# Performance work log

Hardware: AMD Instinct MI355X
Metric: run time of the kernel (lower is better)

Reference implementation:

```python
import jax, jax.numpy as jnp
import numpy as np

NUM_HEADS = 12
HEAD_SIZE = 64  # hidden_size // num_heads


def setup_inputs() -> dict:
    key = jax.random.key(0)
    ks = jax.random.split(key, 4)
    B, S, H = 2, 2048, 768
    return {
        "hidden_states": jax.random.normal(ks[0], (B, S, H), dtype=jnp.float32),
        "attention_mask": jnp.ones((B, S), dtype=jnp.int32),
        "Wq": jax.random.normal(ks[1], (H, H), dtype=jnp.float32) * 0.02,
        "bq": jnp.zeros((H,), dtype=jnp.float32),
        "Wk": jax.random.normal(ks[2], (H, H), dtype=jnp.float32) * 0.02,
        "bk": jnp.zeros((H,), dtype=jnp.float32),
        "Wv": jax.random.normal(ks[3], (H, H), dtype=jnp.float32) * 0.02,
        "bv": jnp.zeros((H,), dtype=jnp.float32),
    }


def reference(hidden_states, attention_mask, Wq, bq, Wk, bk, Wv, bv):
    B, S, H = hidden_states.shape
    nh, hs = NUM_HEADS, HEAD_SIZE

    def to_heads(x):  # [B,S,H] -> [nh,B,S,hs] (matches to_multi_head)
        return x.reshape(B, S, nh, hs).transpose(2, 0, 1, 3)

    # torch Linear: y = x @ W.T + b
    q = to_heads(hidden_states @ Wq.T + bq)
    k = to_heads(hidden_states @ Wk.T + bk)
    v = to_heads(hidden_states @ Wv.T + bv)

    scores = jnp.einsum("hbqd,hbkd->hbqk", q, k) / jnp.float32(hs) ** 0.5
    # mask: 1 -> attend, 0 -> -inf; broadcast over query dim
    m = 1.0 - attention_mask.astype(scores.dtype)
    add = jnp.where(m != 0.0, -jnp.inf, 0.0)[None, :, None, :]  # [1,B,1,S]
    probs = jax.nn.softmax(scores + add, axis=-1)
    # dropout is identity in eval mode
    out = jnp.einsum("hbqk,hbkd->hbqd", probs, v)
    # from_multi_head: [nh,B,S,hs] -> [B,S,H]
    return out.transpose(1, 2, 0, 3).reshape(B, S, H)
```

## Files before the change

### kernel.cpp

```cpp
#include <hip/hip_runtime.h>
#include <hip/hip_bf16.h>

#define BATCH 2
#define SEQ   2048
#define HID   768
#define NH    12
#define HS    64
#define MROWS (BATCH*SEQ)
#define N3    (3*HID)
#define HB    (NH*BATCH)

typedef __attribute__((ext_vector_type(8))) short short8;
typedef __attribute__((ext_vector_type(4))) float floatx4;

#define QSCALE 0.1803368801111204f

__device__ __forceinline__ unsigned short f2bf(float x){
  __hip_bfloat16 h = __float2bfloat16(x);
  return __builtin_bit_cast(unsigned short, h);
}
__device__ __forceinline__ unsigned int f2bf2(float lo, float hi){
  return (unsigned int)f2bf(lo) | ((unsigned int)f2bf(hi) << 16);
}
__device__ __forceinline__ void glds16(const unsigned short* g, unsigned short* l){
  __builtin_amdgcn_global_load_lds(
    (const __attribute__((address_space(1))) unsigned int*)g,
    (__attribute__((address_space(3))) unsigned int*)l, 16, 0, 0);
}
#define WAITCNT_VM_LGKM0() __builtin_amdgcn_s_waitcnt(0x0070)

__global__ void f2bf_all_kernel(const float* __restrict__ X,
                                const float* __restrict__ Wq,
                                const float* __restrict__ Wk,
                                const float* __restrict__ Wv,
                                const int* __restrict__ mask,
                                unsigned short* __restrict__ Xb,
                                unsigned short* __restrict__ Wb,
                                float* __restrict__ maskaddG,
                                unsigned int* __restrict__ flagsG){
  const int XQ = MROWS*HID/4;
  const int WQ = HID*HID/4;
  const int NB = (XQ + 3*WQ)/256;
  const int tid = threadIdx.x;
  if(blockIdx.x == NB){
    for(int i=tid;i<BATCH*SEQ;i+=256) maskaddG[i] = mask[i] ? 0.f : -1e30f;
    if(tid < 2) flagsG[tid] = 0u;
    __syncthreads();
    if(tid < BATCH*32){
      int b = tid >> 5, t = tid & 31;
      const int* mrow = mask + b*SEQ + t*64;
      int any = 0;
      for(int i=0;i<64;i++) any |= (mrow[i]==0);
      if(any) atomicOr(&flagsG[b], 1u << t);
    }
    return;
  }
  int i = blockIdx.x * 256 + tid;
  const float* src; unsigned short* dst; int off;
  if(i < XQ){ src = X; dst = Xb; off = i; }
  else {
    int j = i - XQ;
    int w = j / WQ; off = j - w*WQ;
    src = (w==0) ? Wq : (w==1) ? Wk : Wv;
    dst = Wb + (size_t)w*HID*HID;
  }
  float4 v = reinterpret_cast<const float4*>(src)[off];
  ushort4 o;
  o.x = f2bf(v.x); o.y = f2bf(v.y); o.z = f2bf(v.z); o.w = f2bf(v.w);
  reinterpret_cast<ushort4*>(dst)[off] = o;
}

__global__ __launch_bounds__(256) void qkv_gemm_kernel(
    const unsigned short* __restrict__ Xb,
    const unsigned short* __restrict__ Wb,
    const float* __restrict__ bq, const float* __restrict__ bk, const float* __restrict__ bv,
    unsigned short* __restrict__ Qb, unsigned short* __restrict__ Kb,
    unsigned short* __restrict__ Vtb)
{
  __shared__ __align__(16) union {
    struct { unsigned short A[2][128][32]; unsigned short B[2][128][32]; } s;
    unsigned short T[4][64][72];
  } u;
  const int m0 = blockIdx.y << 7;
  const int n0 = blockIdx.x << 7;
  const int tid  = threadIdx.x;
  const int wave = tid >> 6, lane = tid & 63;
  const int wr = wave >> 1, wc = wave & 1;
  const int quad = lane >> 4, l15 = lane & 15;

  const unsigned short* gsrc[4];
  unsigned short* ldst[4];
  #pragma unroll
  for(int p=0;p<4;p++){
    int ck  = ((p&1)<<8) + tid;
    int row = ck>>2, c = ck&3, pc = c ^ (row&3);
    if(p<2){ gsrc[p] = Xb + (size_t)(m0+row)*HID + (pc<<3); ldst[p] = &u.s.A[0][row][c<<3]; }
    else   { gsrc[p] = Wb + (size_t)(n0+row)*HID + (pc<<3); ldst[p] = &u.s.B[0][row][c<<3]; }
  }

  floatx4 acc[4][4];
  #pragma unroll
  for(int i=0;i<4;i++)
    #pragma unroll
    for(int j=0;j<4;j++) acc[i][j] = (floatx4){0.f,0.f,0.f,0.f};

  auto stage = [&](int buf, int k0){
    const int bo = buf*(128*32);
    #pragma unroll
    for(int p=0;p<4;p++) glds16(gsrc[p] + k0, ldst[p] + bo);
  };

  stage(0, 0);
  __syncthreads();

  const int swa = l15 & 3;
  for(int t=0;t<HID/32;t++){
    const int buf = t & 1;
    if(t < HID/32 - 1) stage(buf^1, (t+1)*32);
    short8 a[4], b[4];
    #pragma unroll
    for(int i=0;i<4;i++)
      a[i] = *reinterpret_cast<const short8*>(&u.s.A[buf][wr*64+i*16+l15][(quad^swa)<<3]);
    #pragma unroll
    for(int j=0;j<4;j++)
      b[j] = *reinterpret_cast<const short8*>(&u.s.B[buf][wc*64+j*16+l15][(quad^swa)<<3]);
    #pragma unroll
    for(int i=0;i<4;i++)
      #pragma unroll
      for(int j=0;j<4;j++)
        acc[i][j] = __builtin_amdgcn_mfma_f32_16x16x32_bf16(a[i], b[j], acc[i][j], 0, 0, 0);
    __syncthreads();
  }

  const int which = n0 / HID;
  const int nbase = n0 - which*HID + wc*64;
  const int head  = nbase >> 6;
  const int b_    = m0 >> 11;
  const int hb    = head*BATCH + b_;
  const int s0    = (m0 & 2047) + wr*64;
  if(which < 2){
    unsigned short* dst = which==0 ? Qb : Kb;
    const float* bias = which==0 ? bq : bk;
    const float scale = which==0 ? QSCALE : 1.0f;
    #pragma unroll
    for(int j=0;j<4;j++){
      const float bb = bias[nbase + j*16 + l15];
      #pragma unroll
      for(int i=0;i<4;i++)
        #pragma unroll
        for(int r=0;r<4;r++)
          u.T[wave][i*16 + quad*4 + r][j*16 + l15] = f2bf((acc[i][j][r] + bb)*scale);
    }
    #pragma unroll
    for(int p=0;p<8;p++){
      const int row = p*8 + (lane>>3), dc = (lane&7)*8;
      uint4 v = *reinterpret_cast<const uint4*>(&u.T[wave][row][dc]);
      *reinterpret_cast<uint4*>(dst + ((size_t)(hb<<11) + s0 + row)*HS + dc) = v;
    }
  } else {
    #pragma unroll
    for(int j=0;j<4;j++){
      const float bb = bv[nbase + j*16 + l15];
      #pragma unroll
      for(int i=0;i<4;i++){
        uint2 pk;
        pk.x = f2bf2(acc[i][j][0]+bb, acc[i][j][1]+bb);
        pk.y = f2bf2(acc[i][j][2]+bb, acc[i][j][3]+bb);
        *reinterpret_cast<uint2*>(&u.T[wave][j*16+l15][i*16 + quad*4]) = pk;
      }
    }
    #pragma unroll
    for(int p=0;p<8;p++){
      const int d = p*8 + (lane>>3), cm = lane & 7;
      uint4 v = *reinterpret_cast<const uint4*>(&u.T[wave][d][cm*8]);
      *reinterpret_cast<uint4*>(Vtb + ((size_t)(hb*HS) + d)*SEQ + s0 + cm*8) = v;
    }
  }
}

__global__ __launch_bounds__(320) void attn_kernel(
    const unsigned short* __restrict__ Qb,
    const unsigned short* __restrict__ Kb,
    const unsigned short* __restrict__ Vtb,
    const float* __restrict__ maskaddG,
    const unsigned int* __restrict__ flagsG,
    float* __restrict__ out)
{
  __shared__ __align__(16) unsigned short Ks2 [2][64][64];
  __shared__ __align__(16) unsigned short Vts2[2][64][64];
  __shared__ __align__(16) unsigned short Ps2 [4][16][68];
  __shared__ int ready[2];
  __shared__ int done[2];

  const int bid = blockIdx.x;
  const int hb = bid >> 5, qt = bid & 31, q0 = qt << 6;
  const int tid = threadIdx.x, wave = tid >> 6, lane = tid & 63;
  const int quad = lane >> 4, l15 = lane & 15;
  const int b_ = hb & 1, head = hb >> 1;
  const int NT = SEQ/64;

  if(tid < 2){ ready[tid] = -1; done[tid] = 0; }
  __syncthreads();

  if(wave == 4){
    const int prow = lane >> 3;
    const int pcol = lane & 7;
    const int ppc  = pcol ^ prow;
    const unsigned short* gK0 = Kb  + ((size_t)(hb<<11) + prow)*HS + (ppc<<3);
    const unsigned short* gV0 = Vtb + ((size_t)(hb*HS) + prow)*SEQ + (ppc<<3);

    for(int t=0;t<NT;t++){
      const int b = t & 1, k0 = t << 6;
      const int k = (t - b) >> 1;
      if(k > 0){
        while(__hip_atomic_load(&done[b], __ATOMIC_ACQUIRE, __HIP_MEMORY_SCOPE_WORKGROUP) < 4*k)
          __builtin_amdgcn_s_sleep(1);
      }
      #pragma unroll
      for(int p=0;p<8;p++)
        glds16(gK0 + (size_t)(k0 + p*8)*HS, &Ks2[b][p*8 + prow][pcol*8]);
      #pragma unroll
      for(int p=0;p<8;p++)
        glds16(gV0 + (size_t)(p*8)*SEQ + k0, &Vts2[b][p*8 + prow][pcol*8]);
      WAITCNT_VM_LGKM0();
      if(lane == 0)
        __hip_atomic_store(&ready[b], t, __ATOMIC_RELEASE, __HIP_MEMORY_SCOPE_WORKGROUP);
    }
    return;
  }

  short8 a_q[2];
  {
    const unsigned short* qsrc = Qb + ((size_t)(hb<<11) + q0 + wave*16 + l15)*HS;
    a_q[0] = *reinterpret_cast<const short8*>(qsrc + quad*8);
    a_q[1] = *reinterpret_cast<const short8*>(qsrc + 32 + quad*8);
  }
  const unsigned int fl = flagsG[b_];

  float lsum4[4] = {0.f,0.f,0.f,0.f};
  floatx4 o_acc[4];
  #pragma unroll
  for(int dt=0;dt<4;dt++) o_acc[dt] = (floatx4){0.f,0.f,0.f,0.f};

  const int sw = l15 & 7;
  for(int t=0;t<NT;t++){
    const int b = t & 1, k0 = t << 6;
    while(__hip_atomic_load(&ready[b], __ATOMIC_ACQUIRE, __HIP_MEMORY_SCOPE_WORKGROUP) < t)
      __builtin_amdgcn_s_sleep(1);

    const unsigned short (*Kst)[64] = Ks2[b];
    const unsigned short (*Vst)[64] = Vts2[b];

    floatx4 st[4];
    #pragma unroll
    for(int kt=0;kt<4;kt++){
      st[kt] = (floatx4){0.f,0.f,0.f,0.f};
      #pragma unroll
      for(int c=0;c<2;c++){
        short8 kf = *reinterpret_cast<const short8*>(
            &Kst[kt*16 + l15][(((c<<2)+quad)^sw)<<3]);
        st[kt] = __builtin_amdgcn_mfma_f32_16x16x32_bf16(kf, a_q[c], st[kt], 0, 0, 0);
      }
    }

    const bool masked = (fl >> t) & 1u;
    #pragma unroll
    for(int kt=0;kt<4;kt++){
      float p0,p1,p2,p3;
      if(!masked){
        p0 = exp2f(st[kt][0]); p1 = exp2f(st[kt][1]);
        p2 = exp2f(st[kt][2]); p3 = exp2f(st[kt][3]);
      } else {
        float4 ma = *reinterpret_cast<const float4*>(
            maskaddG + (b_<<11) + k0 + kt*16 + quad*4);
        p0 = exp2f(st[kt][0] + ma.x); p1 = exp2f(st[kt][1] + ma.y);
        p2 = exp2f(st[kt][2] + ma.z); p3 = exp2f(st[kt][3] + ma.w);
      }
      lsum4[0] += p0; lsum4[1] += p1; lsum4[2] += p2; lsum4[3] += p3;
      uint2 pk;
      pk.x = f2bf2(p0, p1);
      pk.y = f2bf2(p2, p3);
      *reinterpret_cast<uint2*>(&Ps2[wave][l15][kt*16 + quad*4]) = pk;
    }

    short8 ap0, ap1;
    {
      unsigned long long x0 = *reinterpret_cast<const unsigned long long*>(&Ps2[wave][l15][quad*8]);
      unsigned long long x1 = *reinterpret_cast<const unsigned long long*>(&Ps2[wave][l15][quad*8 + 4]);
      unsigned long long y0 = *reinterpret_cast<const unsigned long long*>(&Ps2[wave][l15][32 + quad*8]);
      unsigned long long y1 = *reinterpret_cast<const unsigned long long*>(&Ps2[wave][l15][32 + quad*8 + 4]);
      union { unsigned long long u[2]; short8 s; } cv0, cv1;
      cv0.u[0] = x0; cv0.u[1] = x1;
      cv1.u[0] = y0; cv1.u[1] = y1;
      ap0 = cv0.s; ap1 = cv1.s;
    }
    #pragma unroll
    for(int dt=0;dt<4;dt++){
      short8 bv0 = *reinterpret_cast<const short8*>(&Vst[dt*16 + l15][(quad^sw)<<3]);
      short8 bv1 = *reinterpret_cast<const short8*>(&Vst[dt*16 + l15][((4+quad)^sw)<<3]);
      o_acc[dt] = __builtin_amdgcn_mfma_f32_16x16x32_bf16(ap0, bv0, o_acc[dt], 0, 0, 0);
      o_acc[dt] = __builtin_amdgcn_mfma_f32_16x16x32_bf16(ap1, bv1, o_acc[dt], 0, 0, 0);
    }

    WAITCNT_VM_LGKM0();
    if(lane == 0)
      __hip_atomic_fetch_add(&done[b], 1, __ATOMIC_RELEASE, __HIP_MEMORY_SCOPE_WORKGROUP);
  }

  float lsum = (lsum4[0]+lsum4[1]) + (lsum4[2]+lsum4[3]);
  lsum += __shfl_xor(lsum, 16);
  lsum += __shfl_xor(lsum, 32);
  float linv[4];
  #pragma unroll
  for(int r=0;r<4;r++) linv[r] = 1.0f / __shfl(lsum, quad*4 + r);

  #pragma unroll
  for(int dt=0;dt<4;dt++){
    #pragma unroll
    for(int r=0;r<4;r++){
      const int srow = q0 + wave*16 + quad*4 + r;
      out[((size_t)(b_<<11) + srow)*HID + (head<<6) + dt*16 + l15] =
        o_acc[dt][r] * linv[r];
    }
  }
}

extern "C" void kernel_launch(void* const* d_in, const int* in_sizes, int n_in,
                              void* d_out, int out_size, void* d_ws, size_t ws_size,
                              hipStream_t stream) {
  const float* X    = (const float*)d_in[0];
  const int*   mask = (const int*)  d_in[1];
  const float* Wq   = (const float*)d_in[2];
  const float* bq   = (const float*)d_in[3];
  const float* Wk   = (const float*)d_in[4];
  const float* bk   = (const float*)d_in[5];
  const float* Wv   = (const float*)d_in[6];
  const float* bv   = (const float*)d_in[7];
  float* out = (float*)d_out;

  char* ws = (char*)d_ws;
  unsigned short* Xb  = (unsigned short*)ws;
  unsigned short* Wb  = Xb  + (size_t)MROWS*HID;
  unsigned short* Qb  = Wb  + (size_t)N3*HID;
  unsigned short* Kb  = Qb  + (size_t)HB*SEQ*HS;
  unsigned short* Vtb = Kb  + (size_t)HB*SEQ*HS;
  float* maskaddG = (float*)(Vtb + (size_t)HB*SEQ*HS);
  unsigned int* flagsG = (unsigned int*)(maskaddG + MROWS);

  const int total_quads = (MROWS*HID + 3*HID*HID)/4;
  f2bf_all_kernel<<<total_quads/256 + 1, 256, 0, stream>>>(
      X, Wq, Wk, Wv, mask, Xb, Wb, maskaddG, flagsG);

  qkv_gemm_kernel<<<dim3(N3/128, MROWS/128), 256, 0, stream>>>(
      Xb, Wb, bq, bk, bv, Qb, Kb, Vtb);

  attn_kernel<<<HB*32, 320, 0, stream>>>(
      Qb, Kb, Vtb, maskaddG, flagsG, out);
}
```

Before: 175.5 us.

## Process two query sub-tiles per consumer wave in attention, halving consumer waves

```diff
diff --git a/kernel.cpp b/kernel.cpp
--- a/kernel.cpp
+++ b/kernel.cpp
@@ -21,6 +21,11 @@
 }
 __device__ __forceinline__ unsigned int f2bf2(float lo, float hi){
   return (unsigned int)f2bf(lo) | ((unsigned int)f2bf(hi) << 16);
+}
+__device__ __forceinline__ unsigned int f2bf2_rhu(float lo, float hi){
+  unsigned int a = __builtin_bit_cast(unsigned int, lo) + 0x8000u;
+  unsigned int b = __builtin_bit_cast(unsigned int, hi) + 0x8000u;
+  return __builtin_amdgcn_perm(b, a, 0x07060302u);
 }
 __device__ __forceinline__ void glds16(const unsigned short* g, unsigned short* l){
   __builtin_amdgcn_global_load_lds(
@@ -178,7 +183,7 @@
   }
 }
 
-__global__ __launch_bounds__(320) void attn_kernel(
+__global__ __launch_bounds__(192) void attn_kernel(
     const unsigned short* __restrict__ Qb,
     const unsigned short* __restrict__ Kb,
     const unsigned short* __restrict__ Vtb,
@@ -198,11 +203,12 @@
   const int quad = lane >> 4, l15 = lane & 15;
   const int b_ = hb & 1, head = hb >> 1;
   const int NT = SEQ/64;
+  const int NCONS = 2;
 
   if(tid < 2){ ready[tid] = -1; done[tid] = 0; }
   __syncthreads();
 
-  if(wave == 4){
+  if(wave == 2){
     const int prow = lane >> 3;
     const int pcol = lane & 7;
     const int ppc  = pcol ^ prow;
@@ -213,7 +219,7 @@
       const int b = t & 1, k0 = t << 6;
       const int k = (t - b) >> 1;
       if(k > 0){
-        while(__hip_atomic_load(&done[b], __ATOMIC_ACQUIRE, __HIP_MEMORY_SCOPE_WORKGROUP) < 4*k)
+        while(__hip_atomic_load(&done[b], __ATOMIC_ACQUIRE, __HIP_MEMORY_SCOPE_WORKGROUP) < NCONS*k)
           __builtin_amdgcn_s_sleep(1);
       }
       #pragma unroll
@@ -229,18 +235,21 @@
     return;
   }
 
-  short8 a_q[2];
-  {
-    const unsigned short* qsrc = Qb + ((size_t)(hb<<11) + q0 + wave*16 + l15)*HS;
-    a_q[0] = *reinterpret_cast<const short8*>(qsrc + quad*8);
-    a_q[1] = *reinterpret_cast<const short8*>(qsrc + 32 + quad*8);
+  short8 a_q[2][2];
+  #pragma unroll
+  for(int h=0;h<2;h++){
+    const unsigned short* qsrc = Qb + ((size_t)(hb<<11) + q0 + wave*32 + h*16 + l15)*HS;
+    a_q[h][0] = *reinterpret_cast<const short8*>(qsrc + quad*8);
+    a_q[h][1] = *reinterpret_cast<const short8*>(qsrc + 32 + quad*8);
   }
   const unsigned int fl = flagsG[b_];
 
-  float lsum4[4] = {0.f,0.f,0.f,0.f};
-  floatx4 o_acc[4];
-  #pragma unroll
-  for(int dt=0;dt<4;dt++) o_acc[dt] = (floatx4){0.f,0.f,0.f,0.f};
+  float lsum4[2][4] = {{0.f,0.f,0.f,0.f},{0.f,0.f,0.f,0.f}};
+  floatx4 o_acc[2][4];
+  #pragma unroll
+  for(int h=0;h<2;h++)
+    #pragma unroll
+    for(int dt=0;dt<4;dt++) o_acc[h][dt] = (floatx4){0.f,0.f,0.f,0.f};
 
   const int sw = l15 & 7;
   for(int t=0;t<NT;t++){
@@ -251,55 +260,65 @@
     const unsigned short (*Kst)[64] = Ks2[b];
     const unsigned short (*Vst)[64] = Vts2[b];
 
-    floatx4 st[4];
-    #pragma unroll
-    for(int kt=0;kt<4;kt++){
-      st[kt] = (floatx4){0.f,0.f,0.f,0.f};
-      #pragma unroll
-      for(int c=0;c<2;c++){
+    floatx4 st[2][4];
+    #pragma unroll
+    for(int h=0;h<2;h++)
+      #pragma unroll
+      for(int kt=0;kt<4;kt++) st[h][kt] = (floatx4){0.f,0.f,0.f,0.f};
+    #pragma unroll
+    for(int c=0;c<2;c++){
+      #pragma unroll
+      for(int kt=0;kt<4;kt++){
         short8 kf = *reinterpret_cast<const short8*>(
             &Kst[kt*16 + l15][(((c<<2)+quad)^sw)<<3]);
-        st[kt] = __builtin_amdgcn_mfma_f32_16x16x32_bf16(kf, a_q[c], st[kt], 0, 0, 0);
+        st[0][kt] = __builtin_amdgcn_mfma_f32_16x16x32_bf16(kf, a_q[0][c], st[0][kt], 0, 0, 0);
+        st[1][kt] = __builtin_amdgcn_mfma_f32_16x16x32_bf16(kf, a_q[1][c], st[1][kt], 0, 0, 0);
       }
     }
 
     const bool masked = (fl >> t) & 1u;
     #pragma unroll
-    for(int kt=0;kt<4;kt++){
-      float p0,p1,p2,p3;
-      if(!masked){
-        p0 = exp2f(st[kt][0]); p1 = exp2f(st[kt][1]);
-        p2 = exp2f(st[kt][2]); p3 = exp2f(st[kt][3]);
-      } else {
-        float4 ma = *reinterpret_cast<const float4*>(
-            maskaddG + (b_<<11) + k0 + kt*16 + quad*4);
-        p0 = exp2f(st[kt][0] + ma.x); p1 = exp2f(st[kt][1] + ma.y);
-        p2 = exp2f(st[kt][2] + ma.z); p3 = exp2f(st[kt][3] + ma.w);
-      }
-      lsum4[0] += p0; lsum4[1] += p1; lsum4[2] += p2; lsum4[3] += p3;
-      uint2 pk;
-      pk.x = f2bf2(p0, p1);
-      pk.y = f2bf2(p2, p3);
-      *reinterpret_cast<uint2*>(&Ps2[wave][l15][kt*16 + quad*4]) = pk;
-    }
-
-    short8 ap0, ap1;
-    {
-      unsigned long long x0 = *reinterpret_cast<const unsigned long long*>(&Ps2[wave][l15][quad*8]);
-      unsigned long long x1 = *reinterpret_cast<const unsigned long long*>(&Ps2[wave][l15][quad*8 + 4]);
-      unsigned long long y0 = *reinterpret_cast<const unsigned long long*>(&Ps2[wave][l15][32 + quad*8]);
-      unsigned long long y1 = *reinterpret_cast<const unsigned long long*>(&Ps2[wave][l15][32 + quad*8 + 4]);
+    for(int h=0;h<2;h++){
+      #pragma unroll
+      for(int kt=0;kt<4;kt++){
+        float p0,p1,p2,p3;
+        if(!masked){
+          p0 = exp2f(st[h][kt][0]); p1 = exp2f(st[h][kt][1]);
+          p2 = exp2f(st[h][kt][2]); p3 = exp2f(st[h][kt][3]);
+        } else {
+          float4 ma = *reinterpret_cast<const float4*>(
+              maskaddG + (b_<<11) + k0 + kt*16 + quad*4);
+          p0 = exp2f(st[h][kt][0] + ma.x); p1 = exp2f(st[h][kt][1] + ma.y);
+          p2 = exp2f(st[h][kt][2] + ma.z); p3 = exp2f(st[h][kt][3] + ma.w);
+        }
+        lsum4[h][0] += p0; lsum4[h][1] += p1; lsum4[h][2] += p2; lsum4[h][3] += p3;
+        uint2 pk;
+        pk.x = f2bf2_rhu(p0, p1);
+        pk.y = f2bf2_rhu(p2, p3);
+        *reinterpret_cast<uint2*>(&Ps2[(wave<<1)+h][l15][kt*16 + quad*4]) = pk;
+      }
+    }
+
+    short8 ap[2][2];
+    #pragma unroll
+    for(int h=0;h<2;h++){
+      unsigned long long x0 = *reinterpret_cast<const unsigned long long*>(&Ps2[(wave<<1)+h][l15][quad*8]);
+      unsigned long long x1 = *reinterpret_cast<const unsigned long long*>(&Ps2[(wave<<1)+h][l15][quad*8 + 4]);
+      unsigned long long y0 = *reinterpret_cast<const unsigned long long*>(&Ps2[(wave<<1)+h][l15][32 + quad*8]);
+      unsigned long long y1 = *reinterpret_cast<const unsigned long long*>(&Ps2[(wave<<1)+h][l15][32 + quad*8 + 4]);
       union { unsigned long long u[2]; short8 s; } cv0, cv1;
       cv0.u[0] = x0; cv0.u[1] = x1;
       cv1.u[0] = y0; cv1.u[1] = y1;
-      ap0 = cv0.s; ap1 = cv1.s;
+      ap[h][0] = cv0.s; ap[h][1] = cv1.s;
     }
     #pragma unroll
     for(int dt=0;dt<4;dt++){
       short8 bv0 = *reinterpret_cast<const short8*>(&Vst[dt*16 + l15][(quad^sw)<<3]);
       short8 bv1 = *reinterpret_cast<const short8*>(&Vst[dt*16 + l15][((4+quad)^sw)<<3]);
-      o_acc[dt] = __builtin_amdgcn_mfma_f32_16x16x32_bf16(ap0, bv0, o_acc[dt], 0, 0, 0);
-      o_acc[dt] = __builtin_amdgcn_mfma_f32_16x16x32_bf16(ap1, bv1, o_acc[dt], 0, 0, 0);
+      o_acc[0][dt] = __builtin_amdgcn_mfma_f32_16x16x32_bf16(ap[0][0], bv0, o_acc[0][dt], 0, 0, 0);
+      o_acc[0][dt] = __builtin_amdgcn_mfma_f32_16x16x32_bf16(ap[0][1], bv1, o_acc[0][dt], 0, 0, 0);
+      o_acc[1][dt] = __builtin_amdgcn_mfma_f32_16x16x32_bf16(ap[1][0], bv0, o_acc[1][dt], 0, 0, 0);
+      o_acc[1][dt] = __builtin_amdgcn_mfma_f32_16x16x32_bf16(ap[1][1], bv1, o_acc[1][dt], 0, 0, 0);
     }
 
     WAITCNT_VM_LGKM0();
@@ -307,20 +326,22 @@
       __hip_atomic_fetch_add(&done[b], 1, __ATOMIC_RELEASE, __HIP_MEMORY_SCOPE_WORKGROUP);
   }
 
-  float lsum = (lsum4[0]+lsum4[1]) + (lsum4[2]+lsum4[3]);
-  lsum += __shfl_xor(lsum, 16);
-  lsum += __shfl_xor(lsum, 32);
-  float linv[4];
-  #pragma unroll
-  for(int r=0;r<4;r++) linv[r] = 1.0f / __shfl(lsum, quad*4 + r);
-
-  #pragma unroll
-  for(int dt=0;dt<4;dt++){
-    #pragma unroll
-    for(int r=0;r<4;r++){
-      const int srow = q0 + wave*16 + quad*4 + r;
-      out[((size_t)(b_<<11) + srow)*HID + (head<<6) + dt*16 + l15] =
-        o_acc[dt][r] * linv[r];
+  #pragma unroll
+  for(int h=0;h<2;h++){
+    float lsum = (lsum4[h][0]+lsum4[h][1]) + (lsum4[h][2]+lsum4[h][3]);
+    lsum += __shfl_xor(lsum, 16);
+    lsum += __shfl_xor(lsum, 32);
+    float linv[4];
+    #pragma unroll
+    for(int r=0;r<4;r++) linv[r] = 1.0f / __shfl(lsum, quad*4 + r);
+    #pragma unroll
+    for(int dt=0;dt<4;dt++){
+      #pragma unroll
+      for(int r=0;r<4;r++){
+        const int srow = q0 + wave*32 + h*16 + quad*4 + r;
+        out[((size_t)(b_<<11) + srow)*HID + (head<<6) + dt*16 + l15] =
+          o_acc[h][dt][r] * linv[r];
+      }
     }
   }
 }
@@ -354,6 +375,6 @@
   qkv_gemm_kernel<<<dim3(N3/128, MROWS/128), 256, 0, stream>>>(
       Xb, Wb, bq, bk, bv, Qb, Kb, Vtb);
 
-  attn_kernel<<<HB*32, 320, 0, stream>>>(
+  attn_kernel<<<HB*32, 192, 0, stream>>>(
       Qb, Kb, Vtb, maskaddG, flagsG, out);
 }
```

Result: slower. 221.4 us (+26.2%).
